# Kernel tuning notes

Hardware: AMD Instinct MI355X
Metric: run time of the kernel (lower is better)

Reference implementation:

```python
import jax, jax.numpy as jnp
import numpy as np

HID = 64
HEADS = 4
HEAD_DIM = HID // HEADS
N_MOL, N_PROT = 2048, 4096
E_MOL, E_PROT = 32768, 131072
B = 32


def _lin(key, din, dout):
    kw, kb = jax.random.split(key)
    s = 1.0 / np.sqrt(din)
    W = jax.random.uniform(kw, (din, dout), jnp.float32, -s, s)
    b = jax.random.uniform(kb, (dout,), jnp.float32, -s, s)
    return W, b


def setup_inputs() -> dict:
    key = jax.random.key(0)
    ks = jax.random.split(key, 32)
    inp = {}
    inp['mol_x'] = jax.random.normal(ks[0], (N_MOL, 11), jnp.float32)
    inp['prot_x'] = jax.random.normal(ks[1], (N_PROT, 15), jnp.float32)
    inp['mol_eattr'] = jax.random.normal(ks[2], (E_MOL, 10), jnp.float32)
    inp['prot_eattr'] = jax.random.normal(ks[3], (E_PROT, 10), jnp.float32)
    inp['mol_edge_index'] = jax.random.randint(ks[4], (2, E_MOL), 0, N_MOL, jnp.int32)
    inp['prot_edge_index'] = jax.random.randint(ks[5], (2, E_PROT), 0, N_PROT, jnp.int32)
    inp['mol_batch'] = jnp.sort(jax.random.randint(ks[6], (N_MOL,), 0, B, jnp.int32))
    inp['prot_batch'] = jnp.sort(jax.random.randint(ks[7], (N_PROT,), 0, B, jnp.int32))
    inp['node_lin_mol_W'], inp['node_lin_mol_b'] = _lin(ks[8], 11, HID)
    inp['node_lin_prot_W'], inp['node_lin_prot_b'] = _lin(ks[9], 15, HID)
    inp['edge_lin_mol_W'], inp['edge_lin_mol_b'] = _lin(ks[10], 10, HID)
    inp['edge_lin_prot_W'], inp['edge_lin_prot_b'] = _lin(ks[11], 10, HID)
    for pref, base in (('mol_conv', 12), ('prot_conv', 15)):
        W1s, b1s, W2s, b2s = [], [], [], []
        for l in range(3):
            k1, k2 = jax.random.split(ks[base + l])
            W1, b1 = _lin(k1, HID, HID)
            W2, b2 = _lin(k2, HID, HID)
            W1s.append(W1); b1s.append(b1); W2s.append(W2); b2s.append(b2)
        inp[pref + '_W1'] = jnp.stack(W1s); inp[pref + '_b1'] = jnp.stack(b1s)
        inp[pref + '_W2'] = jnp.stack(W2s); inp[pref + '_b2'] = jnp.stack(b2s)
    for pref, base in (('attn_mp', 18), ('attn_pm', 21)):
        Ws, bs = [], []
        for i in range(3):  # Q, K, V
            W, b = _lin(ks[base + i], HID, HID)
            Ws.append(W); bs.append(b)
        inp[pref + '_W'] = jnp.stack(Ws); inp[pref + '_b'] = jnp.stack(bs)
    inp['fc1_W'], inp['fc1_b'] = _lin(ks[24], 2 * HID, HID)
    inp['fc2_W'], inp['fc2_b'] = _lin(ks[25], HID, 1)
    return inp


def _gine_layer(x, src, dst, eattr, W1, b1, W2, b2):
    # message: ReLU(x_j + e_ji); GINEConv sum aggregation; eps = 0
    msg = jax.nn.relu(x[src] + eattr)                       # [E, H]
    agg = jax.ops.segment_sum(msg, dst, num_segments=x.shape[0])
    h = x + agg
    h = jax.nn.relu(h @ W1 + b1) @ W2 + b2                  # inner MLP
    return jax.nn.relu(h)                                   # post-conv ReLU


def _cross_attn(qn, kn, W, b):
    Nq, Nk = qn.shape[0], kn.shape[0]
    Q = (qn @ W[0] + b[0]).reshape(Nq, HEADS, HEAD_DIM)
    K = (kn @ W[1] + b[1]).reshape(Nk, HEADS, HEAD_DIM)
    V = (kn @ W[2] + b[2]).reshape(Nk, HEADS, HEAD_DIM)
    scores = jnp.einsum('qhd,khd->hqk', Q, K) / np.sqrt(HEAD_DIM)
    w = jax.nn.softmax(scores, axis=-1)
    out = jnp.einsum('hqk,khd->qhd', w, V)
    return out.reshape(Nq, HID)


def _pool(H, batch):
    s = jax.ops.segment_sum(H, batch, num_segments=B)
    c = jax.ops.segment_sum(jnp.ones((H.shape[0],), H.dtype), batch, num_segments=B)
    return s / jnp.maximum(c, 1.0)[:, None]


def _forward(mol_x, prot_x, mol_eattr, prot_eattr,
             node_lin_mol_W, node_lin_mol_b, node_lin_prot_W, node_lin_prot_b,
             edge_lin_mol_W, edge_lin_mol_b, edge_lin_prot_W, edge_lin_prot_b,
             mol_conv_W1, mol_conv_b1, mol_conv_W2, mol_conv_b2,
             prot_conv_W1, prot_conv_b1, prot_conv_W2, prot_conv_b2,
             attn_mp_W, attn_mp_b, attn_pm_W, attn_pm_b,
             fc1_W, fc1_b, fc2_W, fc2_b,
             mol_edge_index, prot_edge_index, mol_batch, prot_batch):
    xm = mol_x @ node_lin_mol_W + node_lin_mol_b
    xp = prot_x @ node_lin_prot_W + node_lin_prot_b
    em = mol_eattr @ edge_lin_mol_W + edge_lin_mol_b
    ep = prot_eattr @ edge_lin_prot_W + edge_lin_prot_b
    ms, md = mol_edge_index[0], mol_edge_index[1]
    ps, pd = prot_edge_index[0], prot_edge_index[1]
    for l in range(3):
        xm = _gine_layer(xm, ms, md, em, mol_conv_W1[l], mol_conv_b1[l], mol_conv_W2[l], mol_conv_b2[l])
    for l in range(3):
        xp = _gine_layer(xp, ps, pd, ep, prot_conv_W1[l], prot_conv_b1[l], prot_conv_W2[l], prot_conv_b2[l])
    H_mol = xm + _cross_attn(xm, xp, attn_mp_W, attn_mp_b)
    H_prot = xp + _cross_attn(xp, xm, attn_pm_W, attn_pm_b)
    z = jnp.concatenate([_pool(H_mol, mol_batch), _pool(H_prot, prot_batch)], axis=1)
    h = jax.nn.relu(z @ fc1_W + fc1_b)
    return jax.nn.sigmoid(h @ fc2_W + fc2_b).squeeze(-1)


def reference(mol_x, prot_x, mol_eattr, prot_eattr,
              node_lin_mol_W, node_lin_mol_b, node_lin_prot_W, node_lin_prot_b,
              edge_lin_mol_W, edge_lin_mol_b, edge_lin_prot_W, edge_lin_prot_b,
              mol_conv_W1, mol_conv_b1, mol_conv_W2, mol_conv_b2,
              prot_conv_W1, prot_conv_b1, prot_conv_W2, prot_conv_b2,
              attn_mp_W, attn_mp_b, attn_pm_W, attn_pm_b,
              fc1_W, fc1_b, fc2_W, fc2_b,
              mol_edge_index, prot_edge_index, mol_batch, prot_batch):
    return _forward(mol_x, prot_x, mol_eattr, prot_eattr,
                    node_lin_mol_W, node_lin_mol_b, node_lin_prot_W, node_lin_prot_b,
                    edge_lin_mol_W, edge_lin_mol_b, edge_lin_prot_W, edge_lin_prot_b,
                    mol_conv_W1, mol_conv_b1, mol_conv_W2, mol_conv_b2,
                    prot_conv_W1, prot_conv_b1, prot_conv_W2, prot_conv_b2,
                    attn_mp_W, attn_mp_b, attn_pm_W, attn_pm_b,
                    fc1_W, fc1_b, fc2_W, fc2_b,
                    mol_edge_index, prot_edge_index, mol_batch, prot_batch)
```

## Files before the change

kernel.cpp:

```cpp
#include <hip/hip_runtime.h>
#include <math.h>

#define HID 64
#define HEADS 4
#define HDIM 16
#define N_MOL 2048
#define N_PROT 4096
#define E_MOL 32768
#define E_PROT 131072
#define BATCH 32
#define N_TOT (N_MOL + N_PROT)
#define E_TOT (E_MOL + E_PROT)
#define CAP 128

#define TQA 16
#define TKA 32
#define KSTA 68
#define CH_MOL 4
#define CH_PROT 2
#define KCHUNK 1024
#define NGRP_MOL (N_MOL / TQA)

#define DOT4(a, b) ((a).x*(b).x + (a).y*(b).y + (a).z*(b).z + (a).w*(b).w)
#define EXP2(x) __builtin_amdgcn_exp2f(x)

__global__ void k_nlb(const float* __restrict__ mol_x, const float* __restrict__ prot_x,
                      const float* __restrict__ Wm, const float* __restrict__ bm,
                      const float* __restrict__ Wp, const float* __restrict__ bp,
                      const int* __restrict__ mol_ei, const int* __restrict__ prot_ei,
                      float* __restrict__ xm, float* __restrict__ xp,
                      int* __restrict__ cursor, int* __restrict__ eidx) {
    if (blockIdx.x < N_TOT / 4) {
        int w = threadIdx.x >> 6, t = threadIdx.x & 63;
        int n = blockIdx.x * 4 + w;
        if (n < N_MOL) {
            const float* xr = mol_x + n * 11;
            float acc = bm[t];
#pragma unroll
            for (int i = 0; i < 11; ++i) acc += xr[i] * Wm[i * HID + t];
            xm[n * HID + t] = acc;
        } else {
            int p = n - N_MOL;
            const float* xr = prot_x + p * 15;
            float acc = bp[t];
#pragma unroll
            for (int i = 0; i < 15; ++i) acc += xr[i] * Wp[i * HID + t];
            xp[p * HID + t] = acc;
        }
    } else {
        int e = (blockIdx.x - N_TOT / 4) * 256 + threadIdx.x;
        int node, loc;
        if (e < E_MOL) { node = mol_ei[E_MOL + e]; loc = e; }
        else { int el = e - E_MOL; node = N_MOL + prot_ei[E_PROT + el]; loc = el; }
        int pos = atomicAdd(&cursor[node], 1);
        eidx[(size_t)node * CAP + pos] = loc;
    }
}

__global__ void k_gine(const float* __restrict__ xin_m, const float* __restrict__ xin_p,
                       float* __restrict__ xout_m, float* __restrict__ xout_p,
                       const float* __restrict__ mol_ea, const float* __restrict__ prot_ea,
                       const int* __restrict__ mol_ei, const int* __restrict__ prot_ei,
                       const float* __restrict__ Wem, const float* __restrict__ bem,
                       const float* __restrict__ Wep, const float* __restrict__ bep,
                       const float* __restrict__ W1m, const float* __restrict__ b1m,
                       const float* __restrict__ W2m, const float* __restrict__ b2m,
                       const float* __restrict__ W1p, const float* __restrict__ b1p,
                       const float* __restrict__ W2p, const float* __restrict__ b2p,
                       const int* __restrict__ cnt, const int* __restrict__ eidx) {
    __shared__ float h0[8][HID];
    __shared__ float h1[8][HID];
    int w = threadIdx.x >> 6, t = threadIdx.x & 63;
    int nb0 = blockIdx.x * 8 + w * 2;
    bool isMol = nb0 < N_MOL;
    const float* x  = isMol ? xin_m : xin_p;
    float* xo       = isMol ? xout_m : xout_p;
    const float* We = isMol ? Wem : Wep;
    float bt        = isMol ? bem[t] : bep[t];
    const float* ea_base = isMol ? mol_ea : prot_ea;
    const int* srcarr    = isMol ? mol_ei : prot_ei;
    int nbias = isMol ? 0 : N_MOL;
    float wcol[10];
#pragma unroll
    for (int i = 0; i < 10; ++i) wcol[i] = We[i * HID + t];

#pragma unroll
    for (int u = 0; u < 2; ++u) {
        int nb = nb0 + u;
        int deg = cnt[nb];
        const int* lst = eidx + (size_t)nb * CAP;
        float agg = 0.f;
        int j = 0;
        for (; j + 1 < deg; j += 2) {
            int e0 = lst[j], e1 = lst[j + 1];
            int s0 = srcarr[e0], s1 = srcarr[e1];
            const float2* p0 = (const float2*)(ea_base + (size_t)e0 * 10);
            const float2* p1 = (const float2*)(ea_base + (size_t)e1 * 10);
            float2 a0 = p0[0], a1 = p0[1], a2 = p0[2], a3 = p0[3], a4 = p0[4];
            float2 c0 = p1[0], c1 = p1[1], c2 = p1[2], c3 = p1[3], c4 = p1[4];
            float xs0 = x[s0 * HID + t];
            float xs1 = x[s1 * HID + t];
            float m0 = bt, m1 = bt;
            m0 = fmaf(a0.x, wcol[0], m0); m0 = fmaf(a0.y, wcol[1], m0);
            m0 = fmaf(a1.x, wcol[2], m0); m0 = fmaf(a1.y, wcol[3], m0);
            m0 = fmaf(a2.x, wcol[4], m0); m0 = fmaf(a2.y, wcol[5], m0);
            m0 = fmaf(a3.x, wcol[6], m0); m0 = fmaf(a3.y, wcol[7], m0);
            m0 = fmaf(a4.x, wcol[8], m0); m0 = fmaf(a4.y, wcol[9], m0);
            m1 = fmaf(c0.x, wcol[0], m1); m1 = fmaf(c0.y, wcol[1], m1);
            m1 = fmaf(c1.x, wcol[2], m1); m1 = fmaf(c1.y, wcol[3], m1);
            m1 = fmaf(c2.x, wcol[4], m1); m1 = fmaf(c2.y, wcol[5], m1);
            m1 = fmaf(c3.x, wcol[6], m1); m1 = fmaf(c3.y, wcol[7], m1);
            m1 = fmaf(c4.x, wcol[8], m1); m1 = fmaf(c4.y, wcol[9], m1);
            agg += fmaxf(m0 + xs0, 0.f) + fmaxf(m1 + xs1, 0.f);
        }
        if (j < deg) {
            int e0 = lst[j];
            int s0 = srcarr[e0];
            const float2* p0 = (const float2*)(ea_base + (size_t)e0 * 10);
            float2 a0 = p0[0], a1 = p0[1], a2 = p0[2], a3 = p0[3], a4 = p0[4];
            float xs0 = x[s0 * HID + t];
            float m0 = bt;
            m0 = fmaf(a0.x, wcol[0], m0); m0 = fmaf(a0.y, wcol[1], m0);
            m0 = fmaf(a1.x, wcol[2], m0); m0 = fmaf(a1.y, wcol[3], m0);
            m0 = fmaf(a2.x, wcol[4], m0); m0 = fmaf(a2.y, wcol[5], m0);
            m0 = fmaf(a3.x, wcol[6], m0); m0 = fmaf(a3.y, wcol[7], m0);
            m0 = fmaf(a4.x, wcol[8], m0); m0 = fmaf(a4.y, wcol[9], m0);
            agg += fmaxf(m0 + xs0, 0.f);
        }
        h0[w * 2 + u][t] = x[(nb0 - nbias + u) * HID + t] + agg;
    }

    const float* W1 = isMol ? W1m : W1p;
    const float* W2 = isMol ? W2m : W2p;
    float b1v = isMol ? b1m[t] : b1p[t];
    float b2v = isMol ? b2m[t] : b2p[t];
    float acc0 = b1v, acc1 = b1v;
    const float4* hA = (const float4*)h0[w * 2];
    const float4* hB = (const float4*)h0[w * 2 + 1];
#pragma unroll
    for (int k = 0; k < 16; ++k) {
        float4 a = hA[k], b = hB[k];
        float w0 = W1[(4 * k + 0) * HID + t], w1 = W1[(4 * k + 1) * HID + t];
        float w2 = W1[(4 * k + 2) * HID + t], w3 = W1[(4 * k + 3) * HID + t];
        acc0 = fmaf(a.x, w0, acc0); acc1 = fmaf(b.x, w0, acc1);
        acc0 = fmaf(a.y, w1, acc0); acc1 = fmaf(b.y, w1, acc1);
        acc0 = fmaf(a.z, w2, acc0); acc1 = fmaf(b.z, w2, acc1);
        acc0 = fmaf(a.w, w3, acc0); acc1 = fmaf(b.w, w3, acc1);
    }
    h1[w * 2][t] = fmaxf(acc0, 0.f);
    h1[w * 2 + 1][t] = fmaxf(acc1, 0.f);
    float d0 = b2v, d1 = b2v;
    const float4* gA = (const float4*)h1[w * 2];
    const float4* gB = (const float4*)h1[w * 2 + 1];
#pragma unroll
    for (int k = 0; k < 16; ++k) {
        float4 a = gA[k], b = gB[k];
        float w0 = W2[(4 * k + 0) * HID + t], w1 = W2[(4 * k + 1) * HID + t];
        float w2 = W2[(4 * k + 2) * HID + t], w3 = W2[(4 * k + 3) * HID + t];
        d0 = fmaf(a.x, w0, d0); d1 = fmaf(b.x, w0, d1);
        d0 = fmaf(a.y, w1, d0); d1 = fmaf(b.y, w1, d1);
        d0 = fmaf(a.z, w2, d0); d1 = fmaf(b.z, w2, d1);
        d0 = fmaf(a.w, w3, d0); d1 = fmaf(b.w, w3, d1);
    }
    int n0 = nb0 - nbias;
    xo[n0 * HID + t] = fmaxf(d0, 0.f);
    xo[(n0 + 1) * HID + t] = fmaxf(d1, 0.f);
}

__global__ void k_qkv(const float* __restrict__ xm, const float* __restrict__ xp,
                      const float* __restrict__ mpW, const float* __restrict__ mpb,
                      const float* __restrict__ pmW, const float* __restrict__ pmb,
                      float* __restrict__ Qm, float* __restrict__ Kp, float* __restrict__ Vp,
                      float* __restrict__ Qp, float* __restrict__ Km, float* __restrict__ Vm) {
    __shared__ float row[8][HID];
    int w = threadIdx.x >> 6, t = threadIdx.x & 63;
    int b0 = blockIdx.x * 8;
    const float *src, *W, *bias;
    float* dst;
    int base;
    if (b0 < 2048)       { base = 0;     src = xm; W = mpW;        bias = mpb;       dst = Qm; }
    else if (b0 < 6144)  { base = 2048;  src = xp; W = mpW + 4096; bias = mpb + 64;  dst = Kp; }
    else if (b0 < 10240) { base = 6144;  src = xp; W = mpW + 8192; bias = mpb + 128; dst = Vp; }
    else if (b0 < 14336) { base = 10240; src = xp; W = pmW;        bias = pmb;       dst = Qp; }
    else if (b0 < 16384) { base = 14336; src = xm; W = pmW + 4096; bias = pmb + 64;  dst = Km; }
    else                 { base = 16384; src = xm; W = pmW + 8192; bias = pmb + 128; dst = Vm; }
    int n0 = b0 - base + w * 2, n1 = n0 + 1;
    row[w * 2][t] = src[n0 * HID + t];
    row[w * 2 + 1][t] = src[n1 * HID + t];
    float acc0 = bias[t], acc1 = acc0;
    const float4* rA = (const float4*)row[w * 2];
    const float4* rB = (const float4*)row[w * 2 + 1];
#pragma unroll
    for (int k = 0; k < 16; ++k) {
        float4 a = rA[k], b = rB[k];
        float w0 = W[(4 * k + 0) * HID + t], w1 = W[(4 * k + 1) * HID + t];
        float w2 = W[(4 * k + 2) * HID + t], w3 = W[(4 * k + 3) * HID + t];
        acc0 = fmaf(a.x, w0, acc0); acc1 = fmaf(b.x, w0, acc1);
        acc0 = fmaf(a.y, w1, acc0); acc1 = fmaf(b.y, w1, acc1);
        acc0 = fmaf(a.z, w2, acc0); acc1 = fmaf(b.z, w2, acc1);
        acc0 = fmaf(a.w, w3, acc0); acc1 = fmaf(b.w, w3, acc1);
    }
    dst[n0 * HID + t] = acc0;
    dst[n1 * HID + t] = acc1;
}

__device__ inline void upd4(float4& A, const float4 v0, const float4 v1,
                            float p0, float p1, float al) {
    A.x = fmaf(p1, v1.x, fmaf(p0, v0.x, A.x * al));
    A.y = fmaf(p1, v1.y, fmaf(p0, v0.y, A.y * al));
    A.z = fmaf(p1, v1.z, fmaf(p0, v0.z, A.z * al));
    A.w = fmaf(p1, v1.w, fmaf(p0, v0.w, A.w * al));
}
__device__ inline void merge4(float4& A, const float4 B, float c1, float c2) {
    A.x = A.x * c1 + B.x * c2;
    A.y = A.y * c1 + B.y * c2;
    A.z = A.z * c1 + B.z * c2;
    A.w = A.w * c1 + B.w * c2;
}
__device__ inline float4 shfl4(const float4 a, int off) {
    float4 r;
    r.x = __shfl_xor(a.x, off, 64); r.y = __shfl_xor(a.y, off, 64);
    r.z = __shfl_xor(a.z, off, 64); r.w = __shfl_xor(a.w, off, 64);
    return r;
}

__global__ __launch_bounds__(256) void k_attn(
    const float* __restrict__ Qm, const float* __restrict__ Kp, const float* __restrict__ Vp,
    const float* __restrict__ Qp, const float* __restrict__ Km, const float* __restrict__ Vm,
    float* __restrict__ part_m, float* __restrict__ part_p) {
    __shared__ float Kl[2][TKA * KSTA];
    __shared__ float Vl[2][TKA * KSTA];

    int t = threadIdx.x;
    const float *Q, *K, *V;
    float* part;
    int q0, chunk, CH;
    {
        int b = blockIdx.x;
        const int MOLB = NGRP_MOL * CH_MOL;
        if (b < MOLB) {
            chunk = b & 3; q0 = (b >> 2) * TQA; CH = CH_MOL;
            Q = Qm; K = Kp; V = Vp; part = part_m;
        } else {
            b -= MOLB;
            chunk = b & 1; q0 = (b >> 1) * TQA; CH = CH_PROT;
            Q = Qp; K = Km; V = Vm; part = part_p;
        }
    }
    int kbeg = chunk * KCHUNK;

    int sub = t & 15, h = (t >> 4) & 3, qg = t >> 6;
    int r0 = t >> 4;
    int c0 = (t & 15) << 2;

    const float sc = 0.25f * 1.44269504088896f;
    float4 q4[4][4];
#pragma unroll
    for (int qq = 0; qq < 4; ++qq) {
        const float4* Qr = (const float4*)(Q + (q0 + qg * 4 + qq) * HID + h * HDIM);
#pragma unroll
        for (int j = 0; j < 4; ++j) {
            float4 v = Qr[j];
            v.x *= sc; v.y *= sc; v.z *= sc; v.w *= sc;
            q4[qq][j] = v;
        }
    }

    float mreg[4], lreg[4];
    float4 A[4][4];
#pragma unroll
    for (int qq = 0; qq < 4; ++qq) {
        mreg[qq] = -INFINITY; lreg[qq] = 0.f;
#pragma unroll
        for (int j = 0; j < 4; ++j) A[qq][j] = (float4){0.f, 0.f, 0.f, 0.f};
    }

    {
        const float4* Kg = (const float4*)(K + kbeg * HID);
        const float4* Vg = (const float4*)(V + kbeg * HID);
        float4 ka = Kg[t], kb = Kg[t + 256];
        float4 va = Vg[t], vb = Vg[t + 256];
        *(float4*)&Kl[0][r0 * KSTA + c0] = ka;
        *(float4*)&Kl[0][(r0 + 16) * KSTA + c0] = kb;
        *(float4*)&Vl[0][r0 * KSTA + c0] = va;
        *(float4*)&Vl[0][(r0 + 16) * KSTA + c0] = vb;
    }
    __syncthreads();

    const int NT = KCHUNK / TKA;
    for (int tile = 0; tile < NT; ++tile) {
        int cur = tile & 1;
        float4 ka, kb, va, vb;
        bool more = (tile + 1) < NT;
        if (more) {
            const float4* Kg = (const float4*)(K + (kbeg + (tile + 1) * TKA) * HID);
            const float4* Vg = (const float4*)(V + (kbeg + (tile + 1) * TKA) * HID);
            ka = Kg[t]; kb = Kg[t + 256];
            va = Vg[t]; vb = Vg[t + 256];
        }

        const float4* Kr0 = (const float4*)&Kl[cur][sub * KSTA + h * HDIM];
        const float4* Kr1 = (const float4*)&Kl[cur][(sub + 16) * KSTA + h * HDIM];
        float4 x0 = Kr0[0], x1 = Kr0[1], x2 = Kr0[2], x3 = Kr0[3];
        float4 y0 = Kr1[0], y1 = Kr1[1], y2 = Kr1[2], y3 = Kr1[3];

        float s0[4], s1[4];
#pragma unroll
        for (int qq = 0; qq < 4; ++qq) {
            s0[qq] = DOT4(x0, q4[qq][0]) + DOT4(x1, q4[qq][1]) + DOT4(x2, q4[qq][2]) + DOT4(x3, q4[qq][3]);
            s1[qq] = DOT4(y0, q4[qq][0]) + DOT4(y1, q4[qq][1]) + DOT4(y2, q4[qq][2]) + DOT4(y3, q4[qq][3]);
        }

        const float4* Vr0 = (const float4*)&Vl[cur][sub * KSTA + h * HDIM];
        const float4* Vr1 = (const float4*)&Vl[cur][(sub + 16) * KSTA + h * HDIM];
        float4 v00 = Vr0[0], v01 = Vr0[1], v02 = Vr0[2], v03 = Vr0[3];
        float4 v10 = Vr1[0], v11 = Vr1[1], v12 = Vr1[2], v13 = Vr1[3];

#pragma unroll
        for (int qq = 0; qq < 4; ++qq) {
            float mn = fmaxf(mreg[qq], fmaxf(s0[qq], s1[qq]));
            float al = EXP2(mreg[qq] - mn);
            float p0 = EXP2(s0[qq] - mn);
            float p1 = EXP2(s1[qq] - mn);
            lreg[qq] = lreg[qq] * al + p0 + p1;
            upd4(A[qq][0], v00, v10, p0, p1, al);
            upd4(A[qq][1], v01, v11, p0, p1, al);
            upd4(A[qq][2], v02, v12, p0, p1, al);
            upd4(A[qq][3], v03, v13, p0, p1, al);
            mreg[qq] = mn;
        }

        if (more) {
            int nxt = cur ^ 1;
            *(float4*)&Kl[nxt][r0 * KSTA + c0] = ka;
            *(float4*)&Kl[nxt][(r0 + 16) * KSTA + c0] = kb;
            *(float4*)&Vl[nxt][r0 * KSTA + c0] = va;
            *(float4*)&Vl[nxt][(r0 + 16) * KSTA + c0] = vb;
        }
        __syncthreads();
    }

#pragma unroll
    for (int off = 1; off < 16; off <<= 1) {
#pragma unroll
        for (int qq = 0; qq < 4; ++qq) {
            float m2 = __shfl_xor(mreg[qq], off, 64);
            float l2 = __shfl_xor(lreg[qq], off, 64);
            float4 B0 = shfl4(A[qq][0], off), B1 = shfl4(A[qq][1], off);
            float4 B2 = shfl4(A[qq][2], off), B3 = shfl4(A[qq][3], off);
            float mn = fmaxf(mreg[qq], m2);
            float c1 = EXP2(mreg[qq] - mn), c2 = EXP2(m2 - mn);
            lreg[qq] = lreg[qq] * c1 + l2 * c2;
            merge4(A[qq][0], B0, c1, c2); merge4(A[qq][1], B1, c1, c2);
            merge4(A[qq][2], B2, c1, c2); merge4(A[qq][3], B3, c1, c2);
            mreg[qq] = mn;
        }
    }

    if (sub == 0) {
#pragma unroll
        for (int qq = 0; qq < 4; ++qq) {
            int qi = q0 + qg * 4 + qq;
            float* pp = part + (size_t)((qi * HEADS + h) * CH + chunk) * 20;
            pp[0] = mreg[qq]; pp[1] = lreg[qq];
            *(float4*)&pp[4] = A[qq][0]; *(float4*)&pp[8] = A[qq][1];
            *(float4*)&pp[12] = A[qq][2]; *(float4*)&pp[16] = A[qq][3];
        }
    }
}

__global__ void k_final(const float* __restrict__ part_m, const float* __restrict__ part_p,
                        const float* __restrict__ xm, const float* __restrict__ xp,
                        const int* __restrict__ mb, const int* __restrict__ pb,
                        const float* __restrict__ fc1W, const float* __restrict__ fc1b,
                        const float* __restrict__ fc2W, const float* __restrict__ fc2b,
                        float* __restrict__ out) {
    __shared__ float sm[64][65];
    __shared__ float z[2 * HID];
    int b = blockIdx.x;
    int t = threadIdx.x;
    int h = t & 3, s = t >> 2;
    int ms, me, ps, pe;
    {
        int lo = 0, hi = N_MOL;
        while (lo < hi) { int mid = (lo + hi) >> 1; if (mb[mid] < b) lo = mid + 1; else hi = mid; }
        ms = lo; lo = ms; hi = N_MOL;
        while (lo < hi) { int mid = (lo + hi) >> 1; if (mb[mid] < b + 1) lo = mid + 1; else hi = mid; }
        me = lo;
        lo = 0; hi = N_PROT;
        while (lo < hi) { int mid = (lo + hi) >> 1; if (pb[mid] < b) lo = mid + 1; else hi = mid; }
        ps = lo; lo = ps; hi = N_PROT;
        while (lo < hi) { int mid = (lo + hi) >> 1; if (pb[mid] < b + 1) lo = mid + 1; else hi = mid; }
        pe = lo;
    }

    {
        float acc[16];
#pragma unroll
        for (int d = 0; d < 16; ++d) acc[d] = 0.f;
        for (int q = ms + s; q < me; q += 64) {
            const float* p0 = part_m + (size_t)(q * HEADS + h) * CH_MOL * 20;
            float mmax = -INFINITY;
#pragma unroll
            for (int c = 0; c < CH_MOL; ++c) mmax = fmaxf(mmax, p0[c * 20]);
            float lsum = 0.f, wgt[CH_MOL];
#pragma unroll
            for (int c = 0; c < CH_MOL; ++c) {
                wgt[c] = EXP2(p0[c * 20] - mmax);
                lsum += p0[c * 20 + 1] * wgt[c];
            }
            float inv = 1.f / lsum;
            const float* Xr = xm + q * HID + h * HDIM;
#pragma unroll
            for (int d = 0; d < 16; ++d) {
                float o = Xr[d];
#pragma unroll
                for (int c = 0; c < CH_MOL; ++c)
                    o = fmaf(p0[c * 20 + 4 + d], wgt[c] * inv, o);
                acc[d] += o;
            }
        }
#pragma unroll
        for (int d = 0; d < 16; ++d) sm[s][h * 16 + d] = acc[d];
    }
    __syncthreads();
    if (t < 64) {
        float sum = 0.f;
        for (int ss = 0; ss < 64; ++ss) sum += sm[ss][t];
        z[t] = sum / fmaxf((float)(me - ms), 1.f);
    }
    __syncthreads();

    {
        float acc[16];
#pragma unroll
        for (int d = 0; d < 16; ++d) acc[d] = 0.f;
        for (int q = ps + s; q < pe; q += 64) {
            const float* p0 = part_p + (size_t)(q * HEADS + h) * CH_PROT * 20;
            float m0 = p0[0], m1 = p0[20];
            float mmax = fmaxf(m0, m1);
            float w0 = EXP2(m0 - mmax), w1 = EXP2(m1 - mmax);
            float inv = 1.f / (p0[1] * w0 + p0[21] * w1);
            w0 *= inv; w1 *= inv;
            const float* Xr = xp + q * HID + h * HDIM;
#pragma unroll
            for (int d = 0; d < 16; ++d)
                acc[d] += Xr[d] + p0[4 + d] * w0 + p0[24 + d] * w1;
        }
#pragma unroll
        for (int d = 0; d < 16; ++d) sm[s][h * 16 + d] = acc[d];
    }
    __syncthreads();
    if (t < 64) {
        float sum = 0.f;
        for (int ss = 0; ss < 64; ++ss) sum += sm[ss][t];
        z[64 + t] = sum / fmaxf((float)(pe - ps), 1.f);
    }
    __syncthreads();

    if (t < 64) {
        float acc = fc1b[t];
        const float4* zv = (const float4*)z;
#pragma unroll
        for (int k = 0; k < 32; ++k) {
            float4 hv = zv[k];
            acc = fmaf(hv.x, fc1W[(4 * k + 0) * 64 + t], acc);
            acc = fmaf(hv.y, fc1W[(4 * k + 1) * 64 + t], acc);
            acc = fmaf(hv.z, fc1W[(4 * k + 2) * 64 + t], acc);
            acc = fmaf(hv.w, fc1W[(4 * k + 3) * 64 + t], acc);
        }
        float hv = fmaxf(acc, 0.f);
        float prod = hv * fc2W[t];
#pragma unroll
        for (int off = 32; off > 0; off >>= 1) prod += __shfl_xor(prod, off, 64);
        if (t == 0) out[b] = 1.f / (1.f + __expf(-(prod + fc2b[0])));
    }
}

extern "C" void kernel_launch(void* const* d_in, const int* in_sizes, int n_in,
                              void* d_out, int out_size, void* d_ws, size_t ws_size,
                              hipStream_t stream) {
    const float* mol_x   = (const float*)d_in[0];
    const float* prot_x  = (const float*)d_in[1];
    const float* mol_ea  = (const float*)d_in[2];
    const float* prot_ea = (const float*)d_in[3];
    const int*   mol_ei  = (const int*)d_in[4];
    const int*   prot_ei = (const int*)d_in[5];
    const int*   mol_b   = (const int*)d_in[6];
    const int*   prot_b  = (const int*)d_in[7];
    const float* nlmW = (const float*)d_in[8];
    const float* nlmb = (const float*)d_in[9];
    const float* nlpW = (const float*)d_in[10];
    const float* nlpb = (const float*)d_in[11];
    const float* elmW = (const float*)d_in[12];
    const float* elmb = (const float*)d_in[13];
    const float* elpW = (const float*)d_in[14];
    const float* elpb = (const float*)d_in[15];
    const float* mcW1 = (const float*)d_in[16];
    const float* mcb1 = (const float*)d_in[17];
    const float* mcW2 = (const float*)d_in[18];
    const float* mcb2 = (const float*)d_in[19];
    const float* pcW1 = (const float*)d_in[20];
    const float* pcb1 = (const float*)d_in[21];
    const float* pcW2 = (const float*)d_in[22];
    const float* pcb2 = (const float*)d_in[23];
    const float* mpW  = (const float*)d_in[24];
    const float* mpb  = (const float*)d_in[25];
    const float* pmW  = (const float*)d_in[26];
    const float* pmb  = (const float*)d_in[27];
    const float* fc1W = (const float*)d_in[28];
    const float* fc1b = (const float*)d_in[29];
    const float* fc2W = (const float*)d_in[30];
    const float* fc2b = (const float*)d_in[31];

    float* ws    = (float*)d_ws;
    float* xa_m  = ws;
    float* xa_p  = xa_m + 131072;
    float* xb_m  = xa_p + 262144;
    float* xb_p  = xb_m + 131072;
    float* Qm    = xb_p + 262144;
    float* Kp    = Qm + 131072;
    float* Vp    = Kp + 262144;
    float* Qp    = Vp + 262144;
    float* Km    = Qp + 262144;
    float* Vm    = Km + 131072;
    float* partm = Vm + 131072;
    float* partp = partm + 655360;
    int* cursor  = (int*)(partp + 655360);
    int* eidx    = (int*)partm;

    hipMemsetAsync(cursor, 0, (size_t)N_TOT * 4, stream);

    k_nlb<<<N_TOT / 4 + E_TOT / 256, 256, 0, stream>>>(
        mol_x, prot_x, nlmW, nlmb, nlpW, nlpb, mol_ei, prot_ei, xa_m, xa_p, cursor, eidx);

    k_gine<<<N_TOT / 8, 256, 0, stream>>>(xa_m, xa_p, xb_m, xb_p, mol_ea, prot_ea, mol_ei, prot_ei,
        elmW, elmb, elpW, elpb,
        mcW1, mcb1, mcW2, mcb2, pcW1, pcb1, pcW2, pcb2, cursor, eidx);
    k_gine<<<N_TOT / 8, 256, 0, stream>>>(xb_m, xb_p, xa_m, xa_p, mol_ea, prot_ea, mol_ei, prot_ei,
        elmW, elmb, elpW, elpb,
        mcW1 + 4096, mcb1 + 64, mcW2 + 4096, mcb2 + 64,
        pcW1 + 4096, pcb1 + 64, pcW2 + 4096, pcb2 + 64, cursor, eidx);
    k_gine<<<N_TOT / 8, 256, 0, stream>>>(xa_m, xa_p, xb_m, xb_p, mol_ea, prot_ea, mol_ei, prot_ei,
        elmW, elmb, elpW, elpb,
        mcW1 + 8192, mcb1 + 128, mcW2 + 8192, mcb2 + 128,
        pcW1 + 8192, pcb1 + 128, pcW2 + 8192, pcb2 + 128, cursor, eidx);

    k_qkv<<<18432 / 8, 256, 0, stream>>>(xb_m, xb_p, mpW, mpb, pmW, pmb, Qm, Kp, Vp, Qp, Km, Vm);
    k_attn<<<NGRP_MOL * CH_MOL + (N_PROT / TQA) * CH_PROT, 256, 0, stream>>>(
        Qm, Kp, Vp, Qp, Km, Vm, partm, partp);

    k_final<<<BATCH, 256, 0, stream>>>(partm, partp, xb_m, xb_p, mol_b, prot_b,
                                       fc1W, fc1b, fc2W, fc2b, (float*)d_out);
}
```

Before: 374.2 us.

## Fuse QKV projection into last GINE layer and parallelize pooling across blocks

```diff
diff --git a/kernel.cpp b/kernel.cpp
--- a/kernel.cpp
+++ b/kernel.cpp
@@ -67,7 +67,12 @@
                        const float* __restrict__ W2m, const float* __restrict__ b2m,
                        const float* __restrict__ W1p, const float* __restrict__ b1p,
                        const float* __restrict__ W2p, const float* __restrict__ b2p,
-                       const int* __restrict__ cnt, const int* __restrict__ eidx) {
+                       const int* __restrict__ cnt, const int* __restrict__ eidx,
+                       int doProj,
+                       const float* __restrict__ mpW, const float* __restrict__ mpb,
+                       const float* __restrict__ pmW, const float* __restrict__ pmb,
+                       float* __restrict__ Qm, float* __restrict__ Kp, float* __restrict__ Vp,
+                       float* __restrict__ Qp, float* __restrict__ Km, float* __restrict__ Vm) {
     __shared__ float h0[8][HID];
     __shared__ float h1[8][HID];
     int w = threadIdx.x >> 6, t = threadIdx.x & 63;
@@ -163,45 +168,43 @@
         d0 = fmaf(a.w, w3, d0); d1 = fmaf(b.w, w3, d1);
     }
     int n0 = nb0 - nbias;
-    xo[n0 * HID + t] = fmaxf(d0, 0.f);
-    xo[(n0 + 1) * HID + t] = fmaxf(d1, 0.f);
-}
-
-__global__ void k_qkv(const float* __restrict__ xm, const float* __restrict__ xp,
-                      const float* __restrict__ mpW, const float* __restrict__ mpb,
-                      const float* __restrict__ pmW, const float* __restrict__ pmb,
-                      float* __restrict__ Qm, float* __restrict__ Kp, float* __restrict__ Vp,
-                      float* __restrict__ Qp, float* __restrict__ Km, float* __restrict__ Vm) {
-    __shared__ float row[8][HID];
-    int w = threadIdx.x >> 6, t = threadIdx.x & 63;
-    int b0 = blockIdx.x * 8;
-    const float *src, *W, *bias;
-    float* dst;
-    int base;
-    if (b0 < 2048)       { base = 0;     src = xm; W = mpW;        bias = mpb;       dst = Qm; }
-    else if (b0 < 6144)  { base = 2048;  src = xp; W = mpW + 4096; bias = mpb + 64;  dst = Kp; }
-    else if (b0 < 10240) { base = 6144;  src = xp; W = mpW + 8192; bias = mpb + 128; dst = Vp; }
-    else if (b0 < 14336) { base = 10240; src = xp; W = pmW;        bias = pmb;       dst = Qp; }
-    else if (b0 < 16384) { base = 14336; src = xm; W = pmW + 4096; bias = pmb + 64;  dst = Km; }
-    else                 { base = 16384; src = xm; W = pmW + 8192; bias = pmb + 128; dst = Vm; }
-    int n0 = b0 - base + w * 2, n1 = n0 + 1;
-    row[w * 2][t] = src[n0 * HID + t];
-    row[w * 2 + 1][t] = src[n1 * HID + t];
-    float acc0 = bias[t], acc1 = acc0;
-    const float4* rA = (const float4*)row[w * 2];
-    const float4* rB = (const float4*)row[w * 2 + 1];
-#pragma unroll
-    for (int k = 0; k < 16; ++k) {
-        float4 a = rA[k], b = rB[k];
-        float w0 = W[(4 * k + 0) * HID + t], w1 = W[(4 * k + 1) * HID + t];
-        float w2 = W[(4 * k + 2) * HID + t], w3 = W[(4 * k + 3) * HID + t];
-        acc0 = fmaf(a.x, w0, acc0); acc1 = fmaf(b.x, w0, acc1);
-        acc0 = fmaf(a.y, w1, acc0); acc1 = fmaf(b.y, w1, acc1);
-        acc0 = fmaf(a.z, w2, acc0); acc1 = fmaf(b.z, w2, acc1);
-        acc0 = fmaf(a.w, w3, acc0); acc1 = fmaf(b.w, w3, acc1);
-    }
-    dst[n0 * HID + t] = acc0;
-    dst[n1 * HID + t] = acc1;
+    float xv0 = fmaxf(d0, 0.f), xv1 = fmaxf(d1, 0.f);
+    xo[n0 * HID + t] = xv0;
+    xo[(n0 + 1) * HID + t] = xv1;
+
+    if (doProj) {
+        h0[w * 2][t] = xv0;
+        h0[w * 2 + 1][t] = xv1;
+        const float *WQ, *bQ, *WK, *bK, *WV, *bV;
+        float *dQ, *dK, *dV;
+        if (isMol) { WQ = mpW;        bQ = mpb;       WK = pmW + 4096; bK = pmb + 64;
+                     WV = pmW + 8192; bV = pmb + 128; dQ = Qm; dK = Km; dV = Vm; }
+        else       { WQ = pmW;        bQ = pmb;       WK = mpW + 4096; bK = mpb + 64;
+                     WV = mpW + 8192; bV = mpb + 128; dQ = Qp; dK = Kp; dV = Vp; }
+        float aQ0 = bQ[t], aQ1 = aQ0;
+        float aK0 = bK[t], aK1 = aK0;
+        float aV0 = bV[t], aV1 = aV0;
+        const float4* rA = (const float4*)h0[w * 2];
+        const float4* rB = (const float4*)h0[w * 2 + 1];
+#pragma unroll
+        for (int k = 0; k < 16; ++k) {
+            float4 a = rA[k], b = rB[k];
+#pragma unroll
+            for (int j = 0; j < 4; ++j) {
+                float av = (j == 0) ? a.x : (j == 1) ? a.y : (j == 2) ? a.z : a.w;
+                float bv = (j == 0) ? b.x : (j == 1) ? b.y : (j == 2) ? b.z : b.w;
+                float wq = WQ[(4 * k + j) * HID + t];
+                float wk = WK[(4 * k + j) * HID + t];
+                float wv = WV[(4 * k + j) * HID + t];
+                aQ0 = fmaf(av, wq, aQ0); aQ1 = fmaf(bv, wq, aQ1);
+                aK0 = fmaf(av, wk, aK0); aK1 = fmaf(bv, wk, aK1);
+                aV0 = fmaf(av, wv, aV0); aV1 = fmaf(bv, wv, aV1);
+            }
+        }
+        dQ[n0 * HID + t] = aQ0; dQ[(n0 + 1) * HID + t] = aQ1;
+        dK[n0 * HID + t] = aK0; dK[(n0 + 1) * HID + t] = aK1;
+        dV[n0 * HID + t] = aV0; dV[(n0 + 1) * HID + t] = aV1;
+    }
 }
 
 __device__ inline void upd4(float4& A, const float4 v0, const float4 v1,
@@ -369,15 +372,12 @@
     }
 }
 
-__global__ void k_final(const float* __restrict__ part_m, const float* __restrict__ part_p,
-                        const float* __restrict__ xm, const float* __restrict__ xp,
-                        const int* __restrict__ mb, const int* __restrict__ pb,
-                        const float* __restrict__ fc1W, const float* __restrict__ fc1b,
-                        const float* __restrict__ fc2W, const float* __restrict__ fc2b,
-                        float* __restrict__ out) {
+__global__ void k_pool(const float* __restrict__ part_m, const float* __restrict__ part_p,
+                       const float* __restrict__ xm, const float* __restrict__ xp,
+                       const int* __restrict__ mb, const int* __restrict__ pb,
+                       float* __restrict__ pool, float* __restrict__ cnt) {
     __shared__ float sm[64][65];
-    __shared__ float z[2 * HID];
-    int b = blockIdx.x;
+    int b = blockIdx.x >> 3, sl = blockIdx.x & 7;
     int t = threadIdx.x;
     int h = t & 3, s = t >> 2;
     int ms, me, ps, pe;
@@ -393,12 +393,13 @@
         while (lo < hi) { int mid = (lo + hi) >> 1; if (pb[mid] < b + 1) lo = mid + 1; else hi = mid; }
         pe = lo;
     }
+    if (sl == 0 && t == 0) { cnt[b * 2] = (float)(me - ms); cnt[b * 2 + 1] = (float)(pe - ps); }
 
     {
         float acc[16];
 #pragma unroll
         for (int d = 0; d < 16; ++d) acc[d] = 0.f;
-        for (int q = ms + s; q < me; q += 64) {
+        for (int q = ms + sl + 8 * s; q < me; q += 8 * 64) {
             const float* p0 = part_m + (size_t)(q * HEADS + h) * CH_MOL * 20;
             float mmax = -INFINITY;
 #pragma unroll
@@ -427,7 +428,7 @@
     if (t < 64) {
         float sum = 0.f;
         for (int ss = 0; ss < 64; ++ss) sum += sm[ss][t];
-        z[t] = sum / fmaxf((float)(me - ms), 1.f);
+        unsafeAtomicAdd(&pool[b * 128 + t], sum);
     }
     __syncthreads();
 
@@ -435,7 +436,7 @@
         float acc[16];
 #pragma unroll
         for (int d = 0; d < 16; ++d) acc[d] = 0.f;
-        for (int q = ps + s; q < pe; q += 64) {
+        for (int q = ps + sl + 8 * s; q < pe; q += 8 * 64) {
             const float* p0 = part_p + (size_t)(q * HEADS + h) * CH_PROT * 20;
             float m0 = p0[0], m1 = p0[20];
             float mmax = fmaxf(m0, m1);
@@ -454,27 +455,35 @@
     if (t < 64) {
         float sum = 0.f;
         for (int ss = 0; ss < 64; ++ss) sum += sm[ss][t];
-        z[64 + t] = sum / fmaxf((float)(pe - ps), 1.f);
-    }
+        unsafeAtomicAdd(&pool[b * 128 + 64 + t], sum);
+    }
+}
+
+__global__ void k_head(const float* __restrict__ pool, const float* __restrict__ cnt,
+                       const float* __restrict__ fc1W, const float* __restrict__ fc1b,
+                       const float* __restrict__ fc2W, const float* __restrict__ fc2b,
+                       float* __restrict__ out) {
+    __shared__ float z[128];
+    int b = blockIdx.x, t = threadIdx.x;
+    float cm = fmaxf(cnt[b * 2 + 0], 1.f), cp = fmaxf(cnt[b * 2 + 1], 1.f);
+    z[t] = pool[b * 128 + t] / cm;
+    z[64 + t] = pool[b * 128 + 64 + t] / cp;
     __syncthreads();
-
-    if (t < 64) {
-        float acc = fc1b[t];
-        const float4* zv = (const float4*)z;
-#pragma unroll
-        for (int k = 0; k < 32; ++k) {
-            float4 hv = zv[k];
-            acc = fmaf(hv.x, fc1W[(4 * k + 0) * 64 + t], acc);
-            acc = fmaf(hv.y, fc1W[(4 * k + 1) * 64 + t], acc);
-            acc = fmaf(hv.z, fc1W[(4 * k + 2) * 64 + t], acc);
-            acc = fmaf(hv.w, fc1W[(4 * k + 3) * 64 + t], acc);
-        }
-        float hv = fmaxf(acc, 0.f);
-        float prod = hv * fc2W[t];
-#pragma unroll
-        for (int off = 32; off > 0; off >>= 1) prod += __shfl_xor(prod, off, 64);
-        if (t == 0) out[b] = 1.f / (1.f + __expf(-(prod + fc2b[0])));
-    }
+    float acc = fc1b[t];
+    const float4* zv = (const float4*)z;
+#pragma unroll
+    for (int k = 0; k < 32; ++k) {
+        float4 hv = zv[k];
+        acc = fmaf(hv.x, fc1W[(4 * k + 0) * 64 + t], acc);
+        acc = fmaf(hv.y, fc1W[(4 * k + 1) * 64 + t], acc);
+        acc = fmaf(hv.z, fc1W[(4 * k + 2) * 64 + t], acc);
+        acc = fmaf(hv.w, fc1W[(4 * k + 3) * 64 + t], acc);
+    }
+    float hv = fmaxf(acc, 0.f);
+    float prod = hv * fc2W[t];
+#pragma unroll
+    for (int off = 32; off > 0; off >>= 1) prod += __shfl_xor(prod, off, 64);
+    if (t == 0) out[b] = 1.f / (1.f + __expf(-(prod + fc2b[0])));
 }
 
 extern "C" void kernel_launch(void* const* d_in, const int* in_sizes, int n_in,
@@ -527,29 +536,33 @@
     float* partm = Vm + 131072;
     float* partp = partm + 655360;
     int* cursor  = (int*)(partp + 655360);
+    float* pool  = (float*)(cursor + N_TOT);
+    float* cnt   = pool + 4096;
     int* eidx    = (int*)partm;
 
-    hipMemsetAsync(cursor, 0, (size_t)N_TOT * 4, stream);
+    hipMemsetAsync(cursor, 0, (size_t)(N_TOT + 4096 + 64) * 4, stream);
 
     k_nlb<<<N_TOT / 4 + E_TOT / 256, 256, 0, stream>>>(
         mol_x, prot_x, nlmW, nlmb, nlpW, nlpb, mol_ei, prot_ei, xa_m, xa_p, cursor, eidx);
 
     k_gine<<<N_TOT / 8, 256, 0, stream>>>(xa_m, xa_p, xb_m, xb_p, mol_ea, prot_ea, mol_ei, prot_ei,
         elmW, elmb, elpW, elpb,
-        mcW1, mcb1, mcW2, mcb2, pcW1, pcb1, pcW2, pcb2, cursor, eidx);
+        mcW1, mcb1, mcW2, mcb2, pcW1, pcb1, pcW2, pcb2, cursor, eidx,
+        0, mpW, mpb, pmW, pmb, Qm, Kp, Vp, Qp, Km, Vm);
     k_gine<<<N_TOT / 8, 256, 0, stream>>>(xb_m, xb_p, xa_m, xa_p, mol_ea, prot_ea, mol_ei, prot_ei,
         elmW, elmb, elpW, elpb,
         mcW1 + 4096, mcb1 + 64, mcW2 + 4096, mcb2 + 64,
-        pcW1 + 4096, pcb1 + 64, pcW2 + 4096, pcb2 + 64, cursor, eidx);
+        pcW1 + 4096, pcb1 + 64, pcW2 + 4096, pcb2 + 64, cursor, eidx,
+        0, mpW, mpb, pmW, pmb, Qm, Kp, Vp, Qp, Km, Vm);
     k_gine<<<N_TOT / 8, 256, 0, stream>>>(xa_m, xa_p, xb_m, xb_p, mol_ea, prot_ea, mol_ei, prot_ei,
         elmW, elmb, elpW, elpb,
         mcW1 + 8192, mcb1 + 128, mcW2 + 8192, mcb2 + 128,
-        pcW1 + 8192, pcb1 + 128, pcW2 + 8192, pcb2 + 128, cursor, eidx);
-
-    k_qkv<<<18432 / 8, 256, 0, stream>>>(xb_m, xb_p, mpW, mpb, pmW, pmb, Qm, Kp, Vp, Qp, Km, Vm);
+        pcW1 + 8192, pcb1 + 128, pcW2 + 8192, pcb2 + 128, cursor, eidx,
+        1, mpW, mpb, pmW, pmb, Qm, Kp, Vp, Qp, Km, Vm);
+
     k_attn<<<NGRP_MOL * CH_MOL + (N_PROT / TQA) * CH_PROT, 256, 0, stream>>>(
         Qm, Kp, Vp, Qp, Km, Vm, partm, partp);
 
-    k_final<<<BATCH, 256, 0, stream>>>(partm, partp, xb_m, xb_p, mol_b, prot_b,
-                                       fc1W, fc1b, fc2W, fc2b, (float*)d_out);
-}
+    k_pool<<<BATCH * 8, 256, 0, stream>>>(partm, partp, xb_m, xb_p, mol_b, prot_b, pool, cnt);
+    k_head<<<BATCH, 64, 0, stream>>>(pool, cnt, fc1W, fc1b, fc2W, fc2b, (float*)d_out);
+}
```

Measured after the change: 371.5 us. No clear change (-0.7%).
